# Kernel tuning notes

Hardware: AMD Instinct MI355X
Metric: run time of the kernel (lower is better)

## Reference

```python
import jax, jax.numpy as jnp
import numpy as np

D_MODEL = 768
STATE_N = 16
BATCH = 8
SEQ = 2048


def setup_inputs() -> dict:
    key = jax.random.key(0)
    ks = jax.random.split(key, 12)
    d, n = D_MODEL, STATE_N
    s = 0.02
    inp = {
        "x": jax.random.normal(ks[0], (BATCH, SEQ, d), dtype=jnp.float32),
        # A_log init as in module: log(arange(1..N)) repeated over d_model
        "A_log": jnp.log(jnp.tile(jnp.arange(1, n + 1, dtype=jnp.float32)[None, :], (d, 1))),
        "D_param": jnp.ones((d,), dtype=jnp.float32),
        "B_proj_w": jax.random.normal(ks[1], (n, d), dtype=jnp.float32) * s,
        "C_proj_w": jax.random.normal(ks[2], (n, d), dtype=jnp.float32) * s,
        "delta_w": jax.random.normal(ks[3], (d, d), dtype=jnp.float32) * s,
        "delta_b": jax.random.normal(ks[4], (d,), dtype=jnp.float32) * s,
        "in_w": jax.random.normal(ks[5], (2 * d, d), dtype=jnp.float32) * s,
        "in_b": jax.random.normal(ks[6], (2 * d,), dtype=jnp.float32) * s,
        "out_w": jax.random.normal(ks[7], (d, d), dtype=jnp.float32) * s,
        "out_b": jax.random.normal(ks[8], (d,), dtype=jnp.float32) * s,
        "conv_w": jax.random.normal(ks[9], (d, 1, 3), dtype=jnp.float32) * s,  # depthwise [D,1,K]
        "conv_b": jax.random.normal(ks[10], (d,), dtype=jnp.float32) * s,
    }
    return inp


def _forward(x, A_log, D_param, B_proj_w, C_proj_w, delta_w, delta_b,
             in_w, in_b, out_w, out_b, conv_w, conv_b):
    A = -jnp.exp(A_log)  # [D, N]
    xz = jnp.einsum("bld,ed->ble", x, in_w) + in_b  # [B, L, 2D]
    x_in, z = jnp.split(xz, 2, axis=-1)
    # depthwise conv1d, padding=1, groups=D (cross-correlation, same as torch)
    x_c = jax.lax.conv_general_dilated(
        jnp.transpose(x_in, (0, 2, 1)), conv_w,
        window_strides=(1,), padding=((1, 1),),
        feature_group_count=x.shape[-1],
        dimension_numbers=("NCH", "OIH", "NCH"))
    x_conv = jnp.transpose(x_c, (0, 2, 1)) + conv_b  # [B, L, D]
    x_conv = jax.nn.silu(x_conv)
    delta = jax.nn.softplus(jnp.einsum("bld,ed->ble", x_conv, delta_w) + delta_b)  # [B,L,D]
    B_sel = jnp.einsum("bld,nd->bln", x_conv, B_proj_w)  # [B, L, N]
    C_sel = jnp.einsum("bld,nd->bln", x_conv, C_proj_w)  # [B, L, N]

    Bsz, L, D = x.shape
    N = A.shape[1]

    def step(h, t_in):
        dt, b_t, c_t, x_t = t_in  # [B,D], [B,N], [B,N], [B,D]
        A_bar = jnp.exp(dt[:, :, None] * A[None, :, :])           # [B,D,N]
        h = A_bar * h + (dt[:, :, None] * b_t[:, None, :]) * x_t[:, :, None]
        y_t = jnp.sum(h * c_t[:, None, :], axis=-1)               # [B,D]
        return h, y_t

    xs = (jnp.transpose(delta, (1, 0, 2)), jnp.transpose(B_sel, (1, 0, 2)),
          jnp.transpose(C_sel, (1, 0, 2)), jnp.transpose(x_conv, (1, 0, 2)))
    h0 = jnp.zeros((Bsz, D, N), dtype=x.dtype)
    _, ys = jax.lax.scan(step, h0, xs)
    y = jnp.transpose(ys, (1, 0, 2))  # [B, L, D]

    y = y + x_conv * D_param[None, None, :]
    y = y * jax.nn.silu(z)
    return jnp.einsum("bld,ed->ble", y, out_w) + out_b


def reference(x, A_log, D_param, B_proj_w, C_proj_w, delta_w, delta_b,
              in_w, in_b, out_w, out_b, conv_w, conv_b):
    return _forward(x, A_log, D_param, B_proj_w, C_proj_w, delta_w, delta_b,
                    in_w, in_b, out_w, out_b, conv_w, conv_b)
```

## Files before the change

### kernel.cpp

```cpp
#include <hip/hip_runtime.h>
#include <hip/hip_bf16.h>

#define D_MODEL 768
#define SEQL    2048
#define BATCH   8
#define NSTATE  16
#define NCHUNK  32
#define TCHUNK  64

typedef __attribute__((ext_vector_type(8))) short short8;
typedef __attribute__((ext_vector_type(4))) float f32x4;

typedef const __attribute__((address_space(1))) unsigned int gas1_t;
typedef __attribute__((address_space(3))) unsigned int las3_t;

__device__ __forceinline__ void gload_lds16(const void* g, void* l) {
  __builtin_amdgcn_global_load_lds((gas1_t*)g, (las3_t*)l, 16, 0, 0);
}

__global__ __launch_bounds__(256) void f32_to_bf16_x4(const float* __restrict__ in,
                                                      __hip_bfloat16* __restrict__ out) {
  int i = (blockIdx.x * 256 + threadIdx.x) * 4;
  float4 v = *(const float4*)(in + i);
  out[i + 0] = __float2bfloat16(v.x);
  out[i + 1] = __float2bfloat16(v.y);
  out[i + 2] = __float2bfloat16(v.z);
  out[i + 3] = __float2bfloat16(v.w);
}

__global__ __launch_bounds__(256) void prep_weights(
    const float* __restrict__ in_w, const float* __restrict__ delta_w,
    const float* __restrict__ Bp, const float* __restrict__ Cp,
    const float* __restrict__ out_w, const float* __restrict__ A_log,
    __hip_bfloat16* __restrict__ w_in, __hip_bfloat16* __restrict__ w_dbc,
    __hip_bfloat16* __restrict__ w_out, float* __restrict__ A2) {
  int i = blockIdx.x * 256 + threadIdx.x;
  if (i < 1536 * 768) { w_in[i] = __float2bfloat16(in_w[i]); return; }
  i -= 1536 * 768;
  if (i < 1024 * 768) {
    int row = i / 768, col = i - row * 768;
    float v;
    if (row < 768)      v = delta_w[row * 768 + col];
    else if (row < 784) v = Bp[(row - 768) * 768 + col];
    else if (row < 800) v = Cp[(row - 784) * 768 + col];
    else                v = 0.f;
    w_dbc[i] = __float2bfloat16(v);
    return;
  }
  i -= 1024 * 768;
  if (i < 768 * 768) { w_out[i] = __float2bfloat16(out_w[i]); return; }
  i -= 768 * 768;
  if (i < 768 * 16) A2[i] = -expf(A_log[i]) * 1.44269504088896f;
}

template <int MODE>
__global__ __launch_bounds__(512) void gemm256(
    const __hip_bfloat16* __restrict__ Amat, const __hip_bfloat16* __restrict__ Bw,
    const float* __restrict__ bias, void* __restrict__ out0,
    void* __restrict__ out1, void* __restrict__ out2,
    const int K, const int gxn) {
  __shared__ char lds[131072];
  const int tid  = threadIdx.x;
  const int lane = tid & 63, wave = tid >> 6;
  const int wr = wave >> 2, wc = wave & 3;

  const int nwg = gridDim.x;
  const int id  = blockIdx.x;
  const int swz = (id & 7) * (nwg >> 3) + (id >> 3);
  const int tm = swz / gxn, tn = swz % gxn;
  const int rowA0 = tm * 256, rowB0 = tn * 256;

  const int srow = tid >> 3;
  const int scol = ((((tid & 7) << 4) ^ ((srow & 7) << 4)) >> 1);
  const __hip_bfloat16* gA = Amat + (size_t)(rowA0 + srow) * K + scol;
  const __hip_bfloat16* gB = Bw   + (size_t)(rowB0 + srow) * K + scol;
  const int ldst = tid << 4;

  const int frow = lane & 15;
  const int fq   = lane >> 4;
  const int fswz = (lane & 7) << 4;
  const int pc0 = ((fq << 4)) ^ fswz;
  const int pc1 = (64 | (fq << 4)) ^ fswz;
  const int aro = (wr * 128 + frow) * 128;
  const int bro = (wc * 64 + frow) * 128;

  f32x4 acc[2][2][4][2];
#pragma unroll
  for (int mh = 0; mh < 2; ++mh)
#pragma unroll
    for (int nh = 0; nh < 2; ++nh)
#pragma unroll
      for (int m = 0; m < 4; ++m)
#pragma unroll
        for (int n = 0; n < 2; ++n) acc[mh][nh][m][n] = (f32x4){0.f, 0.f, 0.f, 0.f};

#define STAGE_A(buf, kt)                                                        \
  {                                                                             \
    const __hip_bfloat16* sp = gA + (size_t)(kt) * 64;                          \
    char* dp = lds + ((buf) << 15) + ldst;                                      \
    _Pragma("unroll") for (int ss = 0; ss < 4; ++ss)                            \
        gload_lds16(sp + (size_t)(ss * 64) * K, dp + ss * 8192);                \
  }
#define STAGE_B(buf, kt)                                                        \
  {                                                                             \
    const __hip_bfloat16* sp = gB + (size_t)(kt) * 64;                          \
    char* dp = lds + 65536 + ((buf) << 15) + ldst;                              \
    _Pragma("unroll") for (int ss = 0; ss < 4; ++ss)                            \
        gload_lds16(sp + (size_t)(ss * 64) * K, dp + ss * 8192);                \
  }

  short8 a[4][2], b[2][2];
#define LOADA(sAp, mh)                                                          \
  {                                                                             \
    _Pragma("unroll") for (int m = 0; m < 4; ++m) {                             \
      const char* p = (sAp) + aro + ((mh)*64 + m * 16) * 128;                   \
      a[m][0] = *(const short8*)(p + pc0);                                      \
      a[m][1] = *(const short8*)(p + pc1);                                      \
    }                                                                           \
  }
#define LOADB(sBp, nh)                                                          \
  {                                                                             \
    _Pragma("unroll") for (int n = 0; n < 2; ++n) {                             \
      const char* p = (sBp) + bro + ((nh)*32 + n * 16) * 128;                   \
      b[n][0] = *(const short8*)(p + pc0);                                      \
      b[n][1] = *(const short8*)(p + pc1);                                      \
    }                                                                           \
  }
#define MMA(mh, nh)                                                             \
  {                                                                             \
    __builtin_amdgcn_s_setprio(1);                                              \
    _Pragma("unroll") for (int m = 0; m < 4; ++m)                               \
    _Pragma("unroll") for (int n = 0; n < 2; ++n)                               \
    _Pragma("unroll") for (int ks = 0; ks < 2; ++ks)                            \
        acc[mh][nh][m][n] = __builtin_amdgcn_mfma_f32_16x16x32_bf16(            \
            a[m][ks], b[n][ks], acc[mh][nh][m][n], 0, 0, 0);                    \
    __builtin_amdgcn_s_setprio(0);                                              \
  }

  STAGE_A(0, 0);
  STAGE_B(0, 0);
  asm volatile("s_waitcnt vmcnt(0)" ::: "memory");
  __builtin_amdgcn_s_barrier();

  const int NT = K >> 6;
  for (int kt = 0; kt < NT; ++kt) {
    const int cur = kt & 1, nxt = cur ^ 1;
    char* sA = lds + (cur << 15);
    char* sB = lds + 65536 + (cur << 15);
    const bool st = (kt + 1 < NT);
    LOADA(sA, 0);
    LOADB(sB, 0);
    if (st) STAGE_A(nxt, kt + 1);
    __builtin_amdgcn_s_barrier();
    MMA(0, 0);
    __builtin_amdgcn_s_barrier();
    LOADB(sB, 1);
    if (st) STAGE_B(nxt, kt + 1);
    __builtin_amdgcn_s_barrier();
    MMA(0, 1);
    __builtin_amdgcn_s_barrier();
    LOADA(sA, 1);
    __builtin_amdgcn_s_barrier();
    MMA(1, 1);
    __builtin_amdgcn_s_barrier();
    LOADB(sB, 0);
    __builtin_amdgcn_s_barrier();
    MMA(1, 0);
    asm volatile("s_waitcnt vmcnt(0)" ::: "memory");
    __builtin_amdgcn_s_barrier();
  }

#pragma unroll
  for (int mh = 0; mh < 2; ++mh)
#pragma unroll
    for (int nh = 0; nh < 2; ++nh)
#pragma unroll
      for (int m = 0; m < 4; ++m)
#pragma unroll
        for (int n = 0; n < 2; ++n) {
          const int grow0 = rowA0 + wr * 128 + mh * 64 + m * 16 + fq * 4;
          const int gcol  = rowB0 + wc * 64 + nh * 32 + n * 16 + frow;
#pragma unroll
          for (int i = 0; i < 4; ++i) {
            const size_t grow = grow0 + i;
            float v = acc[mh][nh][m][n][i];
            if (MODE == 0) {
              v += bias[gcol];
              if (gcol < 768)
                ((__hip_bfloat16*)out0)[grow * 768 + gcol] = __float2bfloat16(v);
              else
                ((__hip_bfloat16*)out1)[grow * 768 + gcol - 768] = __float2bfloat16(v);
            } else if (MODE == 1) {
              if (gcol < 768) {
                v += bias[gcol];
                float sp = (v > 20.f) ? v : log1pf(expf(v));
                ((float*)out0)[grow * 768 + gcol] = sp;
              } else if (gcol < 784) {
                ((float*)out1)[grow * 16 + (gcol - 768)] = v;
              } else if (gcol < 800) {
                ((float*)out2)[grow * 16 + (gcol - 784)] = v;
              }
            } else {
              ((float*)out0)[grow * 768 + gcol] = v + bias[gcol];
            }
          }
        }
#undef STAGE_A
#undef STAGE_B
#undef LOADA
#undef LOADB
#undef MMA
}

__global__ __launch_bounds__(256) void conv_silu(
    const __hip_bfloat16* __restrict__ xin, const float* __restrict__ conv_w,
    const float* __restrict__ conv_b, __hip_bfloat16* __restrict__ xc) {
  const int idx = blockIdx.x * 256 + threadIdx.x;
  const int d = idx % 768;
  const int t = (idx / 768) % SEQL;
  const float w0 = conv_w[d * 3], w1 = conv_w[d * 3 + 1], w2 = conv_w[d * 3 + 2];
  float acc = conv_b[d];
  float xm = (t > 0)        ? __bfloat162float(xin[idx - 768]) : 0.f;
  float x0 = __bfloat162float(xin[idx]);
  float xp = (t < SEQL - 1) ? __bfloat162float(xin[idx + 768]) : 0.f;
  acc += w0 * xm + w1 * x0 + w2 * xp;
  const float sig = 1.f / (1.f + __expf(-acc));
  xc[idx] = __float2bfloat16(acc * sig);
}

__global__ __launch_bounds__(256) void scan_pass1(
    const float* __restrict__ delta, const __hip_bfloat16* __restrict__ xconv,
    const float* __restrict__ Bsel, const float* __restrict__ A2,
    float* __restrict__ sumdt, float* __restrict__ Sbuf) {
  const int d = blockIdx.x * 256 + threadIdx.x;
  const int b = blockIdx.y, c = blockIdx.z;
  __shared__ float sB[TCHUNK * 16];
  ((float4*)sB)[threadIdx.x] =
      ((const float4*)(Bsel + ((size_t)b * SEQL + c * TCHUNK) * 16))[threadIdx.x];
  __syncthreads();

  float a2[16];
#pragma unroll
  for (int n = 0; n < 16; ++n) a2[n] = A2[d * 16 + n];
  float h[16] = {};
  float sdt = 0.f;
  const size_t base = ((size_t)b * SEQL + c * TCHUNK) * 768 + d;
  for (int t = 0; t < TCHUNK; ++t) {
    const float dt = delta[base + (size_t)t * 768];
    const float x = __bfloat162float(xconv[base + (size_t)t * 768]);
    sdt += dt;
    const float dtx = dt * x;
    const float* Br = &sB[t * 16];
#pragma unroll
    for (int n = 0; n < 16; ++n) {
      const float a = exp2f(dt * a2[n]);
      h[n] = fmaf(a, h[n], dtx * Br[n]);
    }
  }
  sumdt[((size_t)b * NCHUNK + c) * 768 + d] = sdt;
#pragma unroll
  for (int n = 0; n < 16; ++n)
    Sbuf[(((size_t)b * NCHUNK + c) * 16 + n) * 768 + d] = h[n];
}

__global__ __launch_bounds__(256) void scan_carry(
    const float* __restrict__ sumdt, const float* __restrict__ Sbuf,
    const float* __restrict__ A2, float* __restrict__ Hin) {
  const int idx = blockIdx.x * 256 + threadIdx.x;
  const int b = idx / 768, d = idx - b * 768;
  float a2[16];
#pragma unroll
  for (int n = 0; n < 16; ++n) a2[n] = A2[d * 16 + n];
  float h[16] = {};
  for (int c = 0; c < NCHUNK; ++c) {
    const size_t hb = ((size_t)b * NCHUNK + c) * 16 * 768 + d;
#pragma unroll
    for (int n = 0; n < 16; ++n) Hin[hb + (size_t)n * 768] = h[n];
    const float sd = sumdt[((size_t)b * NCHUNK + c) * 768 + d];
#pragma unroll
    for (int n = 0; n < 16; ++n) {
      const float P = exp2f(sd * a2[n]);
      h[n] = fmaf(P, h[n], Sbuf[hb + (size_t)n * 768]);
    }
  }
}

__global__ __launch_bounds__(256) void scan_pass3(
    const float* __restrict__ delta, const __hip_bfloat16* __restrict__ xconv,
    const __hip_bfloat16* __restrict__ zb, const float* __restrict__ Bsel,
    const float* __restrict__ Csel, const float* __restrict__ A2,
    const float* __restrict__ Hin, const float* __restrict__ Dp,
    __hip_bfloat16* __restrict__ yg) {
  const int d = blockIdx.x * 256 + threadIdx.x;
  const int b = blockIdx.y, c = blockIdx.z;
  __shared__ float sB[TCHUNK * 16], sC[TCHUNK * 16];
  {
    const size_t off = ((size_t)b * SEQL + c * TCHUNK) * 16;
    ((float4*)sB)[threadIdx.x] = ((const float4*)(Bsel + off))[threadIdx.x];
    ((float4*)sC)[threadIdx.x] = ((const float4*)(Csel + off))[threadIdx.x];
  }
  __syncthreads();

  float a2[16];
#pragma unroll
  for (int n = 0; n < 16; ++n) a2[n] = A2[d * 16 + n];
  float h[16];
  {
    const size_t hb = ((size_t)b * NCHUNK + c) * 16 * 768 + d;
#pragma unroll
    for (int n = 0; n < 16; ++n) h[n] = Hin[hb + (size_t)n * 768];
  }
  const float Dpd = Dp[d];
  const size_t base = ((size_t)b * SEQL + c * TCHUNK) * 768 + d;
  for (int t = 0; t < TCHUNK; ++t) {
    const float dt = delta[base + (size_t)t * 768];
    const float x = __bfloat162float(xconv[base + (size_t)t * 768]);
    const float dtx = dt * x;
    const float* Br = &sB[t * 16];
    const float* Cr = &sC[t * 16];
    float y = 0.f;
#pragma unroll
    for (int n = 0; n < 16; ++n) {
      const float a = exp2f(dt * a2[n]);
      h[n] = fmaf(a, h[n], dtx * Br[n]);
      y = fmaf(h[n], Cr[n], y);
    }
    const float z = __bfloat162float(zb[base + (size_t)t * 768]);
    const float sig = 1.f / (1.f + __expf(-z));
    const float out = (y + x * Dpd) * (z * sig);
    yg[base + (size_t)t * 768] = __float2bfloat16(out);
  }
}

extern "C" void kernel_launch(void* const* d_in, const int* in_sizes, int n_in,
                              void* d_out, int out_size, void* d_ws, size_t ws_size,
                              hipStream_t stream) {
  const float* x       = (const float*)d_in[0];
  const float* A_log   = (const float*)d_in[1];
  const float* D_param = (const float*)d_in[2];
  const float* B_proj  = (const float*)d_in[3];
  const float* C_proj  = (const float*)d_in[4];
  const float* delta_w = (const float*)d_in[5];
  const float* delta_b = (const float*)d_in[6];
  const float* in_w    = (const float*)d_in[7];
  const float* in_b    = (const float*)d_in[8];
  const float* out_w   = (const float*)d_in[9];
  const float* out_b   = (const float*)d_in[10];
  const float* conv_w  = (const float*)d_in[11];
  const float* conv_b  = (const float*)d_in[12];

  char* ws = (char*)d_ws;
  __hip_bfloat16* xb      = (__hip_bfloat16*)(ws + 0);
  __hip_bfloat16* w_in_b  = (__hip_bfloat16*)(ws + 25165824);
  __hip_bfloat16* w_dbc_b = (__hip_bfloat16*)(ws + 27525120);
  __hip_bfloat16* w_out_b = (__hip_bfloat16*)(ws + 29097984);
  float*          A2      = (float*)(ws + 30277632);
  __hip_bfloat16* xin_b   = (__hip_bfloat16*)(ws + 30326784);
  __hip_bfloat16* z_b     = (__hip_bfloat16*)(ws + 55492608);
  __hip_bfloat16* xconv_b = (__hip_bfloat16*)(ws + 80658432);
  float*          delta_f = (float*)(ws + 105824256);
  float*          Bsel    = (float*)(ws + 156155904);
  float*          Csel    = (float*)(ws + 157204480);
  float*          sumdt   = (float*)(ws + 158253056);
  float*          Sbuf    = (float*)(ws + 159039488);
  float*          Hin     = (float*)(ws + 171622400);
  __hip_bfloat16* yg      = xb;

  const int BLD = BATCH * SEQL * D_MODEL;

  f32_to_bf16_x4<<<BLD / 4 / 256, 256, 0, stream>>>(x, xb);
  prep_weights<<<(1536 * 768 + 1024 * 768 + 768 * 768 + 768 * 16) / 256, 256, 0, stream>>>(
      in_w, delta_w, B_proj, C_proj, out_w, A_log, w_in_b, w_dbc_b, w_out_b, A2);
  gemm256<0><<<384, 512, 0, stream>>>(xb, w_in_b, in_b, xin_b, z_b, nullptr, 768, 6);
  conv_silu<<<BLD / 256, 256, 0, stream>>>(xin_b, conv_w, conv_b, xconv_b);
  gemm256<1><<<256, 512, 0, stream>>>(xconv_b, w_dbc_b, delta_b, delta_f, Bsel, Csel, 768, 4);
  scan_pass1<<<dim3(3, BATCH, NCHUNK), 256, 0, stream>>>(delta_f, xconv_b, Bsel, A2, sumdt, Sbuf);
  scan_carry<<<24, 256, 0, stream>>>(sumdt, Sbuf, A2, Hin);
  scan_pass3<<<dim3(3, BATCH, NCHUNK), 256, 0, stream>>>(delta_f, xconv_b, z_b, Bsel, Csel, A2,
                                                         Hin, D_param, yg);
  gemm256<2><<<192, 512, 0, stream>>>(yg, w_out_b, out_b, (float*)d_out, nullptr, nullptr, 768, 3);
}
```

Before: 399.0 us.

## Shrink GEMM tiles to 128, store delta as bf16, parallelize carry scan

The 256x256 GEMM with 512 threads is replaced by a 128x128 tile kernel with 256 threads and two blocks per CU, so the small GEMMs launch more workgroups and fill the GPU better. The DBC weight padding drops from 1024 to 896 rows. Delta is now stored as bf16 instead of fp32, which halves its write and read traffic in the scan passes at some cost in precision. The chunk-carry scan gets one thread per (batch, d, n) instead of one per (batch, d), and the x conversion is merged into the weight-prep kernel to save a launch.

```diff
diff --git a/kernel.cpp b/kernel.cpp
--- a/kernel.cpp
+++ b/kernel.cpp
@@ -18,26 +18,28 @@
   __builtin_amdgcn_global_load_lds((gas1_t*)g, (las3_t*)l, 16, 0, 0);
 }
 
-__global__ __launch_bounds__(256) void f32_to_bf16_x4(const float* __restrict__ in,
-                                                      __hip_bfloat16* __restrict__ out) {
-  int i = (blockIdx.x * 256 + threadIdx.x) * 4;
-  float4 v = *(const float4*)(in + i);
-  out[i + 0] = __float2bfloat16(v.x);
-  out[i + 1] = __float2bfloat16(v.y);
-  out[i + 2] = __float2bfloat16(v.z);
-  out[i + 3] = __float2bfloat16(v.w);
-}
-
-__global__ __launch_bounds__(256) void prep_weights(
-    const float* __restrict__ in_w, const float* __restrict__ delta_w,
-    const float* __restrict__ Bp, const float* __restrict__ Cp,
-    const float* __restrict__ out_w, const float* __restrict__ A_log,
-    __hip_bfloat16* __restrict__ w_in, __hip_bfloat16* __restrict__ w_dbc,
-    __hip_bfloat16* __restrict__ w_out, float* __restrict__ A2) {
+__global__ __launch_bounds__(256) void prep_all(
+    const float* __restrict__ x, const float* __restrict__ in_w,
+    const float* __restrict__ delta_w, const float* __restrict__ Bp,
+    const float* __restrict__ Cp, const float* __restrict__ out_w,
+    const float* __restrict__ A_log,
+    __hip_bfloat16* __restrict__ xb, __hip_bfloat16* __restrict__ w_in,
+    __hip_bfloat16* __restrict__ w_dbc, __hip_bfloat16* __restrict__ w_out,
+    float* __restrict__ A2) {
   int i = blockIdx.x * 256 + threadIdx.x;
+  if (i < 3145728) {
+    int j = i * 4;
+    float4 v = *(const float4*)(x + j);
+    xb[j + 0] = __float2bfloat16(v.x);
+    xb[j + 1] = __float2bfloat16(v.y);
+    xb[j + 2] = __float2bfloat16(v.z);
+    xb[j + 3] = __float2bfloat16(v.w);
+    return;
+  }
+  i -= 3145728;
   if (i < 1536 * 768) { w_in[i] = __float2bfloat16(in_w[i]); return; }
   i -= 1536 * 768;
-  if (i < 1024 * 768) {
+  if (i < 896 * 768) {
     int row = i / 768, col = i - row * 768;
     float v;
     if (row < 768)      v = delta_w[row * 768 + col];
@@ -47,28 +49,27 @@
     w_dbc[i] = __float2bfloat16(v);
     return;
   }
-  i -= 1024 * 768;
+  i -= 896 * 768;
   if (i < 768 * 768) { w_out[i] = __float2bfloat16(out_w[i]); return; }
   i -= 768 * 768;
-  if (i < 768 * 16) A2[i] = -expf(A_log[i]) * 1.44269504088896f;
+  A2[i] = -expf(A_log[i]) * 1.44269504088896f;
 }
 
 template <int MODE>
-__global__ __launch_bounds__(512) void gemm256(
+__global__ __launch_bounds__(256, 2) void gemm128(
     const __hip_bfloat16* __restrict__ Amat, const __hip_bfloat16* __restrict__ Bw,
     const float* __restrict__ bias, void* __restrict__ out0,
     void* __restrict__ out1, void* __restrict__ out2,
     const int K, const int gxn) {
-  __shared__ char lds[131072];
+  __shared__ char lds[65536];
   const int tid  = threadIdx.x;
   const int lane = tid & 63, wave = tid >> 6;
-  const int wr = wave >> 2, wc = wave & 3;
-
-  const int nwg = gridDim.x;
-  const int id  = blockIdx.x;
+  const int wr = wave >> 1, wc = wave & 1;
+
+  const int nwg = gridDim.x, id = blockIdx.x;
   const int swz = (id & 7) * (nwg >> 3) + (id >> 3);
-  const int tm = swz / gxn, tn = swz % gxn;
-  const int rowA0 = tm * 256, rowB0 = tn * 256;
+  const int tm = swz / gxn, tn = swz - tm * gxn;
+  const int rowA0 = tm * 128, rowB0 = tn * 128;
 
   const int srow = tid >> 3;
   const int scol = ((((tid & 7) << 4) ^ ((srow & 7) << 4)) >> 1);
@@ -76,44 +77,38 @@
   const __hip_bfloat16* gB = Bw   + (size_t)(rowB0 + srow) * K + scol;
   const int ldst = tid << 4;
 
-  const int frow = lane & 15;
-  const int fq   = lane >> 4;
-  const int fswz = (lane & 7) << 4;
-  const int pc0 = ((fq << 4)) ^ fswz;
+  const int frow = lane & 15, fq = lane >> 4;
+  const int fswz = (frow & 7) << 4;
+  const int pc0 = (fq << 4) ^ fswz;
   const int pc1 = (64 | (fq << 4)) ^ fswz;
-  const int aro = (wr * 128 + frow) * 128;
-  const int bro = (wc * 64 + frow) * 128;
-
-  f32x4 acc[2][2][4][2];
-#pragma unroll
-  for (int mh = 0; mh < 2; ++mh)
-#pragma unroll
-    for (int nh = 0; nh < 2; ++nh)
-#pragma unroll
-      for (int m = 0; m < 4; ++m)
-#pragma unroll
-        for (int n = 0; n < 2; ++n) acc[mh][nh][m][n] = (f32x4){0.f, 0.f, 0.f, 0.f};
-
-#define STAGE_A(buf, kt)                                                        \
+  const int aro = (wr * 64 + frow) << 7;
+  const int bro = (wc * 64 + frow) << 7;
+
+  f32x4 acc[4][4];
+#pragma unroll
+  for (int m = 0; m < 4; ++m)
+#pragma unroll
+    for (int n = 0; n < 4; ++n) acc[m][n] = (f32x4){0.f, 0.f, 0.f, 0.f};
+
+#define SA(buf) (lds + ((buf) << 15))
+#define SB(buf) (lds + ((buf) << 15) + 16384)
+#define STAGE(buf, kt)                                                          \
   {                                                                             \
-    const __hip_bfloat16* sp = gA + (size_t)(kt) * 64;                          \
-    char* dp = lds + ((buf) << 15) + ldst;                                      \
+    const __hip_bfloat16* spA = gA + (size_t)(kt) * 64;                         \
+    const __hip_bfloat16* spB = gB + (size_t)(kt) * 64;                         \
+    char* dA = SA(buf) + ldst;                                                  \
+    char* dB = SB(buf) + ldst;                                                  \
     _Pragma("unroll") for (int ss = 0; ss < 4; ++ss)                            \
-        gload_lds16(sp + (size_t)(ss * 64) * K, dp + ss * 8192);                \
-  }
-#define STAGE_B(buf, kt)                                                        \
-  {                                                                             \
-    const __hip_bfloat16* sp = gB + (size_t)(kt) * 64;                          \
-    char* dp = lds + 65536 + ((buf) << 15) + ldst;                              \
+        gload_lds16(spA + (size_t)(ss * 32) * K, dA + ss * 4096);               \
     _Pragma("unroll") for (int ss = 0; ss < 4; ++ss)                            \
-        gload_lds16(sp + (size_t)(ss * 64) * K, dp + ss * 8192);                \
+        gload_lds16(spB + (size_t)(ss * 32) * K, dB + ss * 4096);               \
   }
 
   short8 a[4][2], b[2][2];
-#define LOADA(sAp, mh)                                                          \
+#define LOADA(sAp)                                                              \
   {                                                                             \
     _Pragma("unroll") for (int m = 0; m < 4; ++m) {                             \
-      const char* p = (sAp) + aro + ((mh)*64 + m * 16) * 128;                   \
+      const char* p = (sAp) + aro + ((m * 16) << 7);                            \
       a[m][0] = *(const short8*)(p + pc0);                                      \
       a[m][1] = *(const short8*)(p + pc1);                                      \
     }                                                                           \
@@ -121,92 +116,78 @@
 #define LOADB(sBp, nh)                                                          \
   {                                                                             \
     _Pragma("unroll") for (int n = 0; n < 2; ++n) {                             \
-      const char* p = (sBp) + bro + ((nh)*32 + n * 16) * 128;                   \
+      const char* p = (sBp) + bro + ((((nh)*2 + n) * 16) << 7);                 \
       b[n][0] = *(const short8*)(p + pc0);                                      \
       b[n][1] = *(const short8*)(p + pc1);                                      \
     }                                                                           \
   }
-#define MMA(mh, nh)                                                             \
+#define MMA(nh)                                                                 \
   {                                                                             \
     __builtin_amdgcn_s_setprio(1);                                              \
     _Pragma("unroll") for (int m = 0; m < 4; ++m)                               \
     _Pragma("unroll") for (int n = 0; n < 2; ++n)                               \
     _Pragma("unroll") for (int ks = 0; ks < 2; ++ks)                            \
-        acc[mh][nh][m][n] = __builtin_amdgcn_mfma_f32_16x16x32_bf16(            \
-            a[m][ks], b[n][ks], acc[mh][nh][m][n], 0, 0, 0);                    \
+        acc[m][(nh)*2 + n] = __builtin_amdgcn_mfma_f32_16x16x32_bf16(           \
+            a[m][ks], b[n][ks], acc[m][(nh)*2 + n], 0, 0, 0);                   \
     __builtin_amdgcn_s_setprio(0);                                              \
   }
 
-  STAGE_A(0, 0);
-  STAGE_B(0, 0);
+  STAGE(0, 0);
   asm volatile("s_waitcnt vmcnt(0)" ::: "memory");
   __builtin_amdgcn_s_barrier();
 
   const int NT = K >> 6;
   for (int kt = 0; kt < NT; ++kt) {
     const int cur = kt & 1, nxt = cur ^ 1;
-    char* sA = lds + (cur << 15);
-    char* sB = lds + 65536 + (cur << 15);
     const bool st = (kt + 1 < NT);
-    LOADA(sA, 0);
-    LOADB(sB, 0);
-    if (st) STAGE_A(nxt, kt + 1);
+    LOADA(SA(cur));
+    LOADB(SB(cur), 0);
+    if (st) STAGE(nxt, kt + 1);
     __builtin_amdgcn_s_barrier();
-    MMA(0, 0);
+    MMA(0);
     __builtin_amdgcn_s_barrier();
-    LOADB(sB, 1);
-    if (st) STAGE_B(nxt, kt + 1);
+    LOADB(SB(cur), 1);
     __builtin_amdgcn_s_barrier();
-    MMA(0, 1);
-    __builtin_amdgcn_s_barrier();
-    LOADA(sA, 1);
-    __builtin_amdgcn_s_barrier();
-    MMA(1, 1);
-    __builtin_amdgcn_s_barrier();
-    LOADB(sB, 0);
-    __builtin_amdgcn_s_barrier();
-    MMA(1, 0);
+    MMA(1);
     asm volatile("s_waitcnt vmcnt(0)" ::: "memory");
     __builtin_amdgcn_s_barrier();
   }
 
 #pragma unroll
-  for (int mh = 0; mh < 2; ++mh)
-#pragma unroll
-    for (int nh = 0; nh < 2; ++nh)
-#pragma unroll
-      for (int m = 0; m < 4; ++m)
-#pragma unroll
-        for (int n = 0; n < 2; ++n) {
-          const int grow0 = rowA0 + wr * 128 + mh * 64 + m * 16 + fq * 4;
-          const int gcol  = rowB0 + wc * 64 + nh * 32 + n * 16 + frow;
-#pragma unroll
-          for (int i = 0; i < 4; ++i) {
-            const size_t grow = grow0 + i;
-            float v = acc[mh][nh][m][n][i];
-            if (MODE == 0) {
-              v += bias[gcol];
-              if (gcol < 768)
-                ((__hip_bfloat16*)out0)[grow * 768 + gcol] = __float2bfloat16(v);
-              else
-                ((__hip_bfloat16*)out1)[grow * 768 + gcol - 768] = __float2bfloat16(v);
-            } else if (MODE == 1) {
-              if (gcol < 768) {
-                v += bias[gcol];
-                float sp = (v > 20.f) ? v : log1pf(expf(v));
-                ((float*)out0)[grow * 768 + gcol] = sp;
-              } else if (gcol < 784) {
-                ((float*)out1)[grow * 16 + (gcol - 768)] = v;
-              } else if (gcol < 800) {
-                ((float*)out2)[grow * 16 + (gcol - 784)] = v;
-              }
-            } else {
-              ((float*)out0)[grow * 768 + gcol] = v + bias[gcol];
-            }
+  for (int m = 0; m < 4; ++m) {
+    const int grow0 = rowA0 + wr * 64 + m * 16 + fq * 4;
+#pragma unroll
+    for (int n = 0; n < 4; ++n) {
+      const int gcol = rowB0 + wc * 64 + n * 16 + frow;
+#pragma unroll
+      for (int i = 0; i < 4; ++i) {
+        const size_t grow = grow0 + i;
+        float v = acc[m][n][i];
+        if (MODE == 0) {
+          v += bias[gcol];
+          if (gcol < 768)
+            ((__hip_bfloat16*)out0)[grow * 768 + gcol] = __float2bfloat16(v);
+          else
+            ((__hip_bfloat16*)out1)[grow * 768 + gcol - 768] = __float2bfloat16(v);
+        } else if (MODE == 1) {
+          if (gcol < 768) {
+            v += bias[gcol];
+            float sp = (v > 20.f) ? v : log1pf(expf(v));
+            ((__hip_bfloat16*)out0)[grow * 768 + gcol] = __float2bfloat16(sp);
+          } else if (gcol < 784) {
+            ((float*)out1)[grow * 16 + (gcol - 768)] = v;
+          } else if (gcol < 800) {
+            ((float*)out2)[grow * 16 + (gcol - 784)] = v;
           }
+        } else {
+          ((float*)out0)[grow * 768 + gcol] = v + bias[gcol];
         }
-#undef STAGE_A
-#undef STAGE_B
+      }
+    }
+  }
+#undef SA
+#undef SB
+#undef STAGE
 #undef LOADA
 #undef LOADB
 #undef MMA
@@ -229,7 +210,7 @@
 }
 
 __global__ __launch_bounds__(256) void scan_pass1(
-    const float* __restrict__ delta, const __hip_bfloat16* __restrict__ xconv,
+    const __hip_bfloat16* __restrict__ delta, const __hip_bfloat16* __restrict__ xconv,
     const float* __restrict__ Bsel, const float* __restrict__ A2,
     float* __restrict__ sumdt, float* __restrict__ Sbuf) {
   const int d = blockIdx.x * 256 + threadIdx.x;
@@ -246,7 +227,7 @@
   float sdt = 0.f;
   const size_t base = ((size_t)b * SEQL + c * TCHUNK) * 768 + d;
   for (int t = 0; t < TCHUNK; ++t) {
-    const float dt = delta[base + (size_t)t * 768];
+    const float dt = __bfloat162float(delta[base + (size_t)t * 768]);
     const float x = __bfloat162float(xconv[base + (size_t)t * 768]);
     sdt += dt;
     const float dtx = dt * x;
@@ -267,26 +248,21 @@
     const float* __restrict__ sumdt, const float* __restrict__ Sbuf,
     const float* __restrict__ A2, float* __restrict__ Hin) {
   const int idx = blockIdx.x * 256 + threadIdx.x;
-  const int b = idx / 768, d = idx - b * 768;
-  float a2[16];
-#pragma unroll
-  for (int n = 0; n < 16; ++n) a2[n] = A2[d * 16 + n];
-  float h[16] = {};
+  const int d = idx % 768;
+  const int n = (idx / 768) & 15;
+  const int b = idx / (768 * 16);
+  const float a2 = A2[d * 16 + n];
+  float h = 0.f;
   for (int c = 0; c < NCHUNK; ++c) {
-    const size_t hb = ((size_t)b * NCHUNK + c) * 16 * 768 + d;
-#pragma unroll
-    for (int n = 0; n < 16; ++n) Hin[hb + (size_t)n * 768] = h[n];
-    const float sd = sumdt[((size_t)b * NCHUNK + c) * 768 + d];
-#pragma unroll
-    for (int n = 0; n < 16; ++n) {
-      const float P = exp2f(sd * a2[n]);
-      h[n] = fmaf(P, h[n], Sbuf[hb + (size_t)n * 768]);
-    }
+    const size_t hb = (((size_t)(b * NCHUNK + c)) * 16 + n) * 768 + d;
+    Hin[hb] = h;
+    const float sd = sumdt[(b * NCHUNK + c) * 768 + d];
+    h = fmaf(exp2f(sd * a2), h, Sbuf[hb]);
   }
 }
 
 __global__ __launch_bounds__(256) void scan_pass3(
-    const float* __restrict__ delta, const __hip_bfloat16* __restrict__ xconv,
+    const __hip_bfloat16* __restrict__ delta, const __hip_bfloat16* __restrict__ xconv,
     const __hip_bfloat16* __restrict__ zb, const float* __restrict__ Bsel,
     const float* __restrict__ Csel, const float* __restrict__ A2,
     const float* __restrict__ Hin, const float* __restrict__ Dp,
@@ -313,7 +289,7 @@
   const float Dpd = Dp[d];
   const size_t base = ((size_t)b * SEQL + c * TCHUNK) * 768 + d;
   for (int t = 0; t < TCHUNK; ++t) {
-    const float dt = delta[base + (size_t)t * 768];
+    const float dt = __bfloat162float(delta[base + (size_t)t * 768]);
     const float x = __bfloat162float(xconv[base + (size_t)t * 768]);
     const float dtx = dt * x;
     const float* Br = &sB[t * 16];
@@ -350,33 +326,32 @@
   const float* conv_b  = (const float*)d_in[12];
 
   char* ws = (char*)d_ws;
-  __hip_bfloat16* xb      = (__hip_bfloat16*)(ws + 0);
-  __hip_bfloat16* w_in_b  = (__hip_bfloat16*)(ws + 25165824);
-  __hip_bfloat16* w_dbc_b = (__hip_bfloat16*)(ws + 27525120);
-  __hip_bfloat16* w_out_b = (__hip_bfloat16*)(ws + 29097984);
-  float*          A2      = (float*)(ws + 30277632);
-  __hip_bfloat16* xin_b   = (__hip_bfloat16*)(ws + 30326784);
-  __hip_bfloat16* z_b     = (__hip_bfloat16*)(ws + 55492608);
-  __hip_bfloat16* xconv_b = (__hip_bfloat16*)(ws + 80658432);
-  float*          delta_f = (float*)(ws + 105824256);
-  float*          Bsel    = (float*)(ws + 156155904);
-  float*          Csel    = (float*)(ws + 157204480);
-  float*          sumdt   = (float*)(ws + 158253056);
-  float*          Sbuf    = (float*)(ws + 159039488);
-  float*          Hin     = (float*)(ws + 171622400);
-  __hip_bfloat16* yg      = xb;
+  __hip_bfloat16* xb       = (__hip_bfloat16*)(ws + 0);
+  __hip_bfloat16* w_in_b   = (__hip_bfloat16*)(ws + 25165824);
+  __hip_bfloat16* w_dbc_b  = (__hip_bfloat16*)(ws + 27525120);
+  __hip_bfloat16* w_out_b  = (__hip_bfloat16*)(ws + 28901376);
+  float*          A2       = (float*)(ws + 30081024);
+  __hip_bfloat16* xin_b    = (__hip_bfloat16*)(ws + 30130176);
+  __hip_bfloat16* z_b      = (__hip_bfloat16*)(ws + 55296000);
+  __hip_bfloat16* xconv_b  = (__hip_bfloat16*)(ws + 80461824);
+  __hip_bfloat16* delta_bf = (__hip_bfloat16*)(ws + 105627648);
+  float*          Bsel     = (float*)(ws + 130793472);
+  float*          Csel     = (float*)(ws + 131842048);
+  float*          sumdt    = (float*)(ws + 132890624);
+  float*          Sbuf     = (float*)(ws + 133677056);
+  float*          Hin      = (float*)(ws + 146259968);
+  __hip_bfloat16* yg       = xb;
 
   const int BLD = BATCH * SEQL * D_MODEL;
 
-  f32_to_bf16_x4<<<BLD / 4 / 256, 256, 0, stream>>>(x, xb);
-  prep_weights<<<(1536 * 768 + 1024 * 768 + 768 * 768 + 768 * 16) / 256, 256, 0, stream>>>(
-      in_w, delta_w, B_proj, C_proj, out_w, A_log, w_in_b, w_dbc_b, w_out_b, A2);
-  gemm256<0><<<384, 512, 0, stream>>>(xb, w_in_b, in_b, xin_b, z_b, nullptr, 768, 6);
+  prep_all<<<21936, 256, 0, stream>>>(x, in_w, delta_w, B_proj, C_proj, out_w, A_log,
+                                      xb, w_in_b, w_dbc_b, w_out_b, A2);
+  gemm128<0><<<1536, 256, 0, stream>>>(xb, w_in_b, in_b, xin_b, z_b, nullptr, 768, 12);
   conv_silu<<<BLD / 256, 256, 0, stream>>>(xin_b, conv_w, conv_b, xconv_b);
-  gemm256<1><<<256, 512, 0, stream>>>(xconv_b, w_dbc_b, delta_b, delta_f, Bsel, Csel, 768, 4);
-  scan_pass1<<<dim3(3, BATCH, NCHUNK), 256, 0, stream>>>(delta_f, xconv_b, Bsel, A2, sumdt, Sbuf);
-  scan_carry<<<24, 256, 0, stream>>>(sumdt, Sbuf, A2, Hin);
-  scan_pass3<<<dim3(3, BATCH, NCHUNK), 256, 0, stream>>>(delta_f, xconv_b, z_b, Bsel, Csel, A2,
+  gemm128<1><<<896, 256, 0, stream>>>(xconv_b, w_dbc_b, delta_b, delta_bf, Bsel, Csel, 768, 7);
+  scan_pass1<<<dim3(3, BATCH, NCHUNK), 256, 0, stream>>>(delta_bf, xconv_b, Bsel, A2, sumdt, Sbuf);
+  scan_carry<<<384, 256, 0, stream>>>(sumdt, Sbuf, A2, Hin);
+  scan_pass3<<<dim3(3, BATCH, NCHUNK), 256, 0, stream>>>(delta_bf, xconv_b, z_b, Bsel, Csel, A2,
                                                          Hin, D_param, yg);
-  gemm256<2><<<192, 512, 0, stream>>>(yg, w_out_b, out_b, (float*)d_out, nullptr, nullptr, 768, 3);
-}
+  gemm128<2><<<768, 256, 0, stream>>>(yg, w_out_b, out_b, (float*)d_out, nullptr, nullptr, 768, 6);
+}
```

New measurement: 383.9 us. 1.04x faster.
